# Optimization experiments

Measured on AMD Instinct MI355X. Metric: run time of the kernel, lower is better.

Reference implementation:

```python
import jax, jax.numpy as jnp
import numpy as np

TWO_N, D = 8192, 256
N = TWO_N // 2


def setup_inputs() -> dict:
    key = jax.random.key(0)
    k1, k2 = jax.random.split(key)
    embeddings = jax.random.normal(k1, (TWO_N, D), dtype=jnp.float32)
    pos_mask = jnp.zeros((N, TWO_N), dtype=bool)  # unused by the loss
    neg_mask = jax.random.randint(k2, (N, TWO_N), 0, 2).astype(bool)
    return {"embeddings": embeddings, "pos_mask": pos_mask, "neg_mask": neg_mask}


def reference(embeddings, pos_mask, neg_mask):
    # d[i, j] = <e_i, e_j>  (other_embeddings defaults to embeddings)
    d = jnp.matmul(embeddings, embeddings.T)            # [2N, 2N]
    n = embeddings.shape[0] // 2
    rows = d[:n]                                        # [N, 2N] (only rows 0..N-1 used)
    ap = rows[jnp.arange(n), jnp.arange(n) + n]         # d[i, i+N], shape [N]
    # masked sum_j exp(d[i,j] - ap_i) over negatives, then log(1 + .)
    expm = jnp.exp(rows - ap[:, None])                  # [N, 2N]
    j_all = jnp.log1p(jnp.sum(jnp.where(neg_mask, expm, 0.0), axis=1))  # [N]
    return jnp.mean(j_all)
```

## Files before the change

### kernel.cpp

```cpp
#include <hip/hip_runtime.h>
#include <math.h>

#define TWO_N 8192
#define NR 4096
#define D 256
#define BM 128
#define BN 128
#define BK 64
#define PMW (TWO_N / 64)

typedef __attribute__((ext_vector_type(8))) short bf16x8;
typedef __attribute__((ext_vector_type(4))) float f32x4;

#define AS1V const __attribute__((address_space(1))) void
#define AS3V __attribute__((address_space(3))) void

__device__ inline unsigned short f2bf(float x) {
  unsigned u = __builtin_bit_cast(unsigned, x);
  u += 0x7fffu + ((u >> 16) & 1u);
  return (unsigned short)(u >> 16);
}

__global__ void cvt_kernel(const float* __restrict__ emb, unsigned short* __restrict__ ebf) {
  const size_t i = ((size_t)blockIdx.x * 256 + threadIdx.x) * 8;
  const float4 a = *reinterpret_cast<const float4*>(emb + i);
  const float4 b = *reinterpret_cast<const float4*>(emb + i + 4);
  union { unsigned short s[8]; bf16x8 v; } o;
  o.s[0] = f2bf(a.x); o.s[1] = f2bf(a.y); o.s[2] = f2bf(a.z); o.s[3] = f2bf(a.w);
  o.s[4] = f2bf(b.x); o.s[5] = f2bf(b.y); o.s[6] = f2bf(b.z); o.s[7] = f2bf(b.w);
  *reinterpret_cast<bf16x8*>(ebf + i) = o.v;
}

__global__ void repack_kernel(const unsigned char* __restrict__ negm,
                              unsigned long long* __restrict__ pm) {
  const int t = blockIdx.x * 256 + threadIdx.x;
  const uint4* p = reinterpret_cast<const uint4*>(negm + (size_t)t * 64);
  unsigned long long w = 0;
#pragma unroll
  for (int q = 0; q < 4; ++q) {
    const uint4 v = p[q];
    unsigned b = 0;
    b |= (v.x & 1u) | ((v.x >> 7) & 2u) | ((v.x >> 14) & 4u) | ((v.x >> 21) & 8u);
    b |= ((v.y & 1u) | ((v.y >> 7) & 2u) | ((v.y >> 14) & 4u) | ((v.y >> 21) & 8u)) << 4;
    b |= ((v.z & 1u) | ((v.z >> 7) & 2u) | ((v.z >> 14) & 4u) | ((v.z >> 21) & 8u)) << 8;
    b |= ((v.w & 1u) | ((v.w >> 7) & 2u) | ((v.w >> 14) & 4u) | ((v.w >> 21) & 8u)) << 12;
    w |= (unsigned long long)b << (q * 16);
  }
  pm[t] = w;
}

__global__ void ap_zero_kernel(const float* __restrict__ emb, float* __restrict__ ap,
                               double* __restrict__ rowsum) {
  const int lane = threadIdx.x & 63;
  const int wid = threadIdx.x >> 6;
  const int i = blockIdx.x * 4 + wid;
  const float4 a = *reinterpret_cast<const float4*>(emb + (size_t)i * D + lane * 4);
  const float4 b = *reinterpret_cast<const float4*>(emb + (size_t)(i + NR) * D + lane * 4);
  float s = a.x * b.x + a.y * b.y + a.z * b.z + a.w * b.w;
#pragma unroll
  for (int off = 32; off >= 1; off >>= 1) s += __shfl_xor(s, off, 64);
  if (lane == 0) { ap[i] = s; rowsum[i] = 0.0; }
}

__global__ __launch_bounds__(256, 2) void fused_mfma(
    const unsigned short* __restrict__ ebf, const unsigned long long* __restrict__ pm,
    const float* __restrict__ ap, double* __restrict__ rowsum) {
  __shared__ unsigned short As[2][BM * BK];
  __shared__ unsigned short Bs[2][BN * BK];
  const int t = threadIdx.x;
  const int lane = t & 63;
  const int wid = t >> 6;
  const int wr = wid >> 1;
  const int wc = wid & 1;
  const int sw = (blockIdx.x & 7) * 256 + (blockIdx.x >> 3);
  const int bi = sw >> 6;
  const int bj = sw & 63;

  f32x4 acc[4][4] = {};

  const int srow = lane >> 3;
  const int scol = (lane & 7) * 8;

  auto STAGE = [&](int buf, int kt) {
    const int k0 = kt * BK;
#pragma unroll
    for (int q = 0; q < 4; ++q) {
      const int rbase = wid * 32 + q * 8;
      const unsigned short* gA = ebf + (size_t)(bi * BM + rbase + srow) * D + k0 + scol;
      const unsigned short* gB = ebf + (size_t)(bj * BN + rbase + srow) * D + k0 + scol;
      __builtin_amdgcn_global_load_lds((AS1V*)gA, (AS3V*)(As[buf] + rbase * BK), 16, 0, 0);
      __builtin_amdgcn_global_load_lds((AS1V*)gB, (AS3V*)(Bs[buf] + rbase * BK), 16, 0, 0);
    }
  };

  STAGE(0, 0);
  __syncthreads();
  int cur = 0;
  for (int kt = 0; kt < D / BK; ++kt) {
    if (kt < D / BK - 1) STAGE(cur ^ 1, kt + 1);
#pragma unroll
    for (int kk = 0; kk < 2; ++kk) {
      bf16x8 af[4], bfr[4];
      const int kof = kk * 32 + (lane >> 4) * 8;
#pragma unroll
      for (int m = 0; m < 4; ++m)
        af[m] = *reinterpret_cast<const bf16x8*>(&As[cur][(wr * 64 + m * 16 + (lane & 15)) * BK + kof]);
#pragma unroll
      for (int n = 0; n < 4; ++n)
        bfr[n] = *reinterpret_cast<const bf16x8*>(&Bs[cur][(wc * 64 + n * 16 + (lane & 15)) * BK + kof]);
#pragma unroll
      for (int m = 0; m < 4; ++m)
#pragma unroll
        for (int n = 0; n < 4; ++n)
          acc[m][n] = __builtin_amdgcn_mfma_f32_16x16x32_bf16(af[m], bfr[n], acc[m][n], 0, 0, 0);
    }
    __syncthreads();
    cur ^= 1;
  }

  const int g = lane >> 4;
  const int cl = lane & 15;
  double rs[4][4] = {};

#pragma unroll
  for (int m = 0; m < 4; ++m) {
    const int rowbase = bi * BM + wr * 64 + m * 16 + g * 4;
#pragma unroll
    for (int r2 = 0; r2 < 4; ++r2) {
      const int row = rowbase + r2;
      const float apv = ap[row];
      const unsigned long long mw = pm[(size_t)row * PMW + bj * 2 + wc];
#pragma unroll
      for (int n = 0; n < 4; ++n) {
        const float x = acc[m][n][r2] - apv;
        const float tt = x * 1.44269504088896340736f;
        const float kf = floorf(tt);
        const float mant = exp2f(tt - kf);
        const long long ebits = (long long)(1023 + (int)kf) << 52;
        const double sc = __builtin_bit_cast(double, ebits);
        const bool msk = (mw >> (n * 16 + cl)) & 1;
        rs[m][r2] += msk ? (double)mant * sc : 0.0;
      }
    }
  }
#pragma unroll
  for (int m = 0; m < 4; ++m)
#pragma unroll
    for (int r2 = 0; r2 < 4; ++r2) {
      double v = rs[m][r2];
#pragma unroll
      for (int off = 8; off >= 1; off >>= 1) v += __shfl_xor(v, off, 64);
      if (cl == 0) atomicAdd(&rowsum[bi * BM + wr * 64 + m * 16 + g * 4 + r2], v);
    }
}

__global__ void finalize_kernel(const double* __restrict__ rowsum, float* __restrict__ out) {
  __shared__ double red[4];
  const int t = threadIdx.x;
  double s = 0.0;
  for (int i = t; i < NR; i += 256) s += log1p(rowsum[i]);
#pragma unroll
  for (int off = 32; off >= 1; off >>= 1) s += __shfl_xor(s, off, 64);
  if ((t & 63) == 0) red[t >> 6] = s;
  __syncthreads();
  if (t == 0) out[0] = (float)((red[0] + red[1] + red[2] + red[3]) * (1.0 / NR));
}

extern "C" void kernel_launch(void* const* d_in, const int* in_sizes, int n_in,
                              void* d_out, int out_size, void* d_ws, size_t ws_size,
                              hipStream_t stream) {
  const float* emb = (const float*)d_in[0];
  const unsigned char* negm = (const unsigned char*)d_in[2];
  float* out = (float*)d_out;
  char* ws = (char*)d_ws;
  unsigned short* ebf = (unsigned short*)ws;
  unsigned long long* pm = (unsigned long long*)(ws + (1u << 22));
  float* ap = (float*)(ws + (2u << 22));
  double* rowsum = (double*)(ws + (2u << 22) + 16384);

  cvt_kernel<<<dim3(TWO_N * D / 8 / 256), dim3(256), 0, stream>>>(emb, ebf);
  repack_kernel<<<dim3(NR * PMW / 256), dim3(256), 0, stream>>>(negm, pm);
  ap_zero_kernel<<<dim3(NR / 4), dim3(256), 0, stream>>>(emb, ap, rowsum);
  fused_mfma<<<dim3((NR / BM) * (TWO_N / BN)), dim3(256), 0, stream>>>(ebf, pm, ap, rowsum);
  finalize_kernel<<<dim3(1), dim3(256), 0, stream>>>(rowsum, out);
}
```

Measured before the change: 328.0 us.

## Prefetch all K tiles upfront with vmcnt-staged waits and XOR-swizzled LDS

Replaces the double-buffered K loop with one up-front issue of all four K-tile async global-to-LDS loads, so the whole 256-wide K dimension is resident in LDS. Each tile's compute starts after a partial s_waitcnt vmcnt and a barrier, letting later tiles' loads overlap earlier tiles' MFMA work. It also XOR-swizzles the 16-byte column chunks in LDS to cut bank conflicts on fragment reads. Using four buffers raises LDS to 128KB per block and drops the two-blocks-per-CU launch bound, which lowers occupancy.

```diff
diff --git a/kernel.cpp b/kernel.cpp
--- a/kernel.cpp
+++ b/kernel.cpp
@@ -7,6 +7,7 @@
 #define BM 128
 #define BN 128
 #define BK 64
+#define NKT 4
 #define PMW (TWO_N / 64)
 
 typedef __attribute__((ext_vector_type(8))) short bf16x8;
@@ -14,6 +15,7 @@
 
 #define AS1V const __attribute__((address_space(1))) void
 #define AS3V __attribute__((address_space(3))) void
+#define WAITVM(n) asm volatile("s_waitcnt vmcnt(" #n ")" ::: "memory")
 
 __device__ inline unsigned short f2bf(float x) {
   unsigned u = __builtin_bit_cast(unsigned, x);
@@ -62,11 +64,11 @@
   if (lane == 0) { ap[i] = s; rowsum[i] = 0.0; }
 }
 
-__global__ __launch_bounds__(256, 2) void fused_mfma(
+__global__ __launch_bounds__(256) void fused_mfma(
     const unsigned short* __restrict__ ebf, const unsigned long long* __restrict__ pm,
     const float* __restrict__ ap, double* __restrict__ rowsum) {
-  __shared__ unsigned short As[2][BM * BK];
-  __shared__ unsigned short Bs[2][BN * BK];
+  __shared__ unsigned short As[NKT][BM * BK];
+  __shared__ unsigned short Bs[NKT][BN * BK];
   const int t = threadIdx.x;
   const int lane = t & 63;
   const int wid = t >> 6;
@@ -79,44 +81,50 @@
   f32x4 acc[4][4] = {};
 
   const int srow = lane >> 3;
-  const int scol = (lane & 7) * 8;
+  const int scol = ((lane & 7) ^ (lane >> 3)) * 8;
 
-  auto STAGE = [&](int buf, int kt) {
+#pragma unroll
+  for (int kt = 0; kt < NKT; ++kt) {
     const int k0 = kt * BK;
 #pragma unroll
     for (int q = 0; q < 4; ++q) {
       const int rbase = wid * 32 + q * 8;
       const unsigned short* gA = ebf + (size_t)(bi * BM + rbase + srow) * D + k0 + scol;
       const unsigned short* gB = ebf + (size_t)(bj * BN + rbase + srow) * D + k0 + scol;
-      __builtin_amdgcn_global_load_lds((AS1V*)gA, (AS3V*)(As[buf] + rbase * BK), 16, 0, 0);
-      __builtin_amdgcn_global_load_lds((AS1V*)gB, (AS3V*)(Bs[buf] + rbase * BK), 16, 0, 0);
+      __builtin_amdgcn_global_load_lds((AS1V*)gA, (AS3V*)(As[kt] + rbase * BK), 16, 0, 0);
+      __builtin_amdgcn_global_load_lds((AS1V*)gB, (AS3V*)(Bs[kt] + rbase * BK), 16, 0, 0);
     }
-  };
+  }
 
-  STAGE(0, 0);
-  __syncthreads();
-  int cur = 0;
-  for (int kt = 0; kt < D / BK; ++kt) {
-    if (kt < D / BK - 1) STAGE(cur ^ 1, kt + 1);
+  const int frow = lane & 15;
+  const int fk = lane >> 4;
+  auto compute_kt = [&](int kt) {
 #pragma unroll
     for (int kk = 0; kk < 2; ++kk) {
       bf16x8 af[4], bfr[4];
-      const int kof = kk * 32 + (lane >> 4) * 8;
+      const int cswz = ((kk * 4 + fk) ^ (lane & 7)) * 8;
 #pragma unroll
       for (int m = 0; m < 4; ++m)
-        af[m] = *reinterpret_cast<const bf16x8*>(&As[cur][(wr * 64 + m * 16 + (lane & 15)) * BK + kof]);
+        af[m] = *reinterpret_cast<const bf16x8*>(&As[kt][(wr * 64 + m * 16 + frow) * BK + cswz]);
 #pragma unroll
       for (int n = 0; n < 4; ++n)
-        bfr[n] = *reinterpret_cast<const bf16x8*>(&Bs[cur][(wc * 64 + n * 16 + (lane & 15)) * BK + kof]);
+        bfr[n] = *reinterpret_cast<const bf16x8*>(&Bs[kt][(wc * 64 + n * 16 + frow) * BK + cswz]);
 #pragma unroll
       for (int m = 0; m < 4; ++m)
 #pragma unroll
         for (int n = 0; n < 4; ++n)
           acc[m][n] = __builtin_amdgcn_mfma_f32_16x16x32_bf16(af[m], bfr[n], acc[m][n], 0, 0, 0);
     }
-    __syncthreads();
-    cur ^= 1;
-  }
+  };
+
+  WAITVM(24); __builtin_amdgcn_s_barrier(); __builtin_amdgcn_sched_barrier(0);
+  compute_kt(0);
+  WAITVM(16); __builtin_amdgcn_s_barrier(); __builtin_amdgcn_sched_barrier(0);
+  compute_kt(1);
+  WAITVM(8);  __builtin_amdgcn_s_barrier(); __builtin_amdgcn_sched_barrier(0);
+  compute_kt(2);
+  WAITVM(0);  __builtin_amdgcn_s_barrier(); __builtin_amdgcn_sched_barrier(0);
+  compute_kt(3);
 
   const int g = lane >> 4;
   const int cl = lane & 15;
```

After: 338.9 us. 1.03x slower.
